# Optimization experiments

Measured on AMD Instinct MI355X. Metric: run time of the kernel, lower is better.

## Reference

```python
import jax, jax.numpy as jnp
import numpy as np

B, L, H = 16, 96, 150
WED, PED = 100, 50
EMB = WED + PED  # 150
WV, TV = 50000, 50


def setup_inputs() -> dict:
    key = jax.random.key(0)
    ks = jax.random.split(key, 16)
    f = lambda k, shape, s=0.1: jax.random.normal(k, shape, dtype=jnp.float32) * s
    return {
        "words_idx_tensor": jax.random.randint(ks[0], (B, L), 0, WV),
        "pos_idx_tensor": jax.random.randint(ks[1], (B, L), 0, TV),
        "max_length": L,
        "word_emb": f(ks[2], (WV, WED)),
        "tag_emb": f(ks[3], (TV, PED)),
        "W_ih0": f(ks[4], (2, 4 * H, EMB)),        # layer 0, both dirs
        "W_ih_rest": f(ks[5], (3, 2, 4 * H, 2 * H)),  # layers 1-3
        "W_hh": f(ks[6], (4, 2, 4 * H, H)),
        "b_ih": f(ks[7], (4, 2, 4 * H)),
        "b_hh": f(ks[8], (4, 2, 4 * H)),
        "w1": jax.random.uniform(ks[9], (1,), jnp.float32, -1.0, 1.0),
        "w2": jax.random.uniform(ks[10], (1,), jnp.float32, -1.0, 1.0),
        "w3": jax.random.uniform(ks[11], (1,), jnp.float32, -1.0, 1.0),
        "w4": jax.random.uniform(ks[12], (1,), jnp.float32, -1.0, 1.0),
        "mlp_w1": f(ks[13], (100, 4 * H)),
        "mlp_b1": jnp.zeros((100,), jnp.float32),
        "mlp_w2": f(ks[14], (1, 100)),
        "mlp_b2": jnp.zeros((1,), jnp.float32),
    }


def _lstm_dir(x, Wih, Whh, bi, bh):
    # x: [B, T, D] -> hidden states [B, T, H]; torch LSTM cell math (gate order i,f,g,o)
    Bx = x.shape[0]
    Hh = Whh.shape[-1]
    pre = jnp.einsum('btd,gd->btg', x, Wih) + bi + bh  # input contribution, [B,T,4H]

    def step(carry, p):
        h, c = carry
        gates = p + h @ Whh.T
        i, fg, g, o = jnp.split(gates, 4, axis=-1)
        i, fg, o = jax.nn.sigmoid(i), jax.nn.sigmoid(fg), jax.nn.sigmoid(o)
        g = jnp.tanh(g)
        c = fg * c + i * g
        h = o * jnp.tanh(c)
        return (h, c), h

    init = (jnp.zeros((Bx, Hh), x.dtype), jnp.zeros((Bx, Hh), x.dtype))
    _, hs = jax.lax.scan(step, init, pre.transpose(1, 0, 2))  # [T,B,H]
    return hs.transpose(1, 0, 2)


def _bilstm(x, W_ih0, W_ih_rest, W_hh, b_ih, b_hh):
    inp = x
    for layer in range(4):  # fixed structural loop over layers
        outs = []
        for d in range(2):  # forward / backward direction
            Wih = W_ih0[d] if layer == 0 else W_ih_rest[layer - 1, d]
            xs = inp if d == 0 else inp[:, ::-1]
            hs = _lstm_dir(xs, Wih, W_hh[layer, d], b_ih[layer, d], b_hh[layer, d])
            outs.append(hs if d == 0 else hs[:, ::-1])
        inp = jnp.concatenate(outs, axis=-1)  # [B,T,2H]
    return inp


def reference(words_idx_tensor, pos_idx_tensor, max_length, word_emb, tag_emb,
              W_ih0, W_ih_rest, W_hh, b_ih, b_hh, w1, w2, w3, w4,
              mlp_w1, mlp_b1, mlp_w2, mlp_b2):
    we = word_emb[words_idx_tensor[:, :max_length]]   # [B,L,WED]
    te = tag_emb[pos_idx_tensor[:, :max_length]]      # [B,L,PED]
    embeds = jnp.concatenate([we, te], axis=-1)       # [B,L,EMB]
    out = _bilstm(embeds, W_ih0, W_ih_rest, W_hh, b_ih, b_hh)  # [B,L,2H]
    Bn, Lm, C = out.shape
    # features[l1, b, l2] = cat(out[b, l1], out[b, l2])  -> [L, B, L, 4H]
    ht = out.transpose(1, 0, 2)  # [L,B,2H]
    head = jnp.broadcast_to(ht[:, :, None, :], (Lm, Bn, Lm, C))
    dep = jnp.broadcast_to(out[None, :, :, :], (Lm, Bn, Lm, C))
    features = jnp.concatenate([head, dep], axis=-1)  # [L,B,L,4H]
    # w1*f + w2*f^2 + w3*f^3 + w4*f^4 via Horner (single fused elementwise pass)
    poly = features * (w1[0] + features * (w2[0] + features * (w3[0] + features * w4[0])))
    h1 = jnp.tanh(poly @ mlp_w1.T + mlp_b1)           # [L,B,L,100]
    edge_scores = h1 @ mlp_w2.T + mlp_b2              # [L,B,L,1]
    return edge_scores
```

## Files before the change

kernel.cpp:

```cpp
#include <hip/hip_runtime.h>

typedef __attribute__((ext_vector_type(8))) _Float16 half8;
typedef __attribute__((ext_vector_type(4))) _Float16 half4;
typedef __attribute__((ext_vector_type(4))) float float4v;

__device__ __forceinline__ float4v mfma16h(half8 a, half8 b, float4v c) {
  return __builtin_amdgcn_mfma_f32_16x16x32_f16(a, b, c, 0, 0, 0);
}

__device__ __forceinline__ half8 cat44h(half4 a, half4 b) {
  half8 r;
  r[0]=a[0]; r[1]=a[1]; r[2]=a[2]; r[3]=a[3];
  r[4]=b[0]; r[5]=b[1]; r[6]=b[2]; r[7]=b[3];
  return r;
}

__device__ __forceinline__ void split_f16(float x, _Float16& hi, _Float16& lo) {
  hi = (_Float16)x;
  lo = (_Float16)(x - (float)hi);
}

#define KLOG2E 1.442695041f
__device__ __forceinline__ float fast_tanh(float x) {
  float z = __builtin_amdgcn_exp2f(2.f * KLOG2E * x);
  return 1.f - 2.f * __builtin_amdgcn_rcpf(1.f + z);
}


__global__ void prep_kernel(
    const float* __restrict__ Wih0,
    const float* __restrict__ WihR,
    const float* __restrict__ Whh,
    const float* __restrict__ bih,
    const float* __restrict__ bhh,
    const float* __restrict__ w1m,
    const float* __restrict__ b1v,
    _Float16* __restrict__ whh_f,
    _Float16* __restrict__ wih_f,
    _Float16* __restrict__ wpr_f,
    float* __restrict__ bsum, float* __restrict__ b1cat)
{
  const int N_whh  = 8 * 40 * 5 * 512;
  const int N_wih0 = 2 * 40 * 5 * 512;
  const int N_wihr = 6 * 40 * 10 * 512;
  const int N_wpr  = 16 * 10 * 512;
  const int N_bs   = 8 * 640;
  const int total  = N_whh + N_wih0 + N_wihr + N_wpr + N_bs + 256;
  for (int i = blockIdx.x * blockDim.x + threadIdx.x; i < total;
       i += gridDim.x * blockDim.x) {
    int idx = i;
    if (idx < N_whh) {
      int e = idx & 7, lane = (idx >> 3) & 63, r = idx >> 9;
      int kc = r % 5; r /= 5; int nt = r % 40; int ld = r / 40;
      int jrow = (nt >> 2) * 16 + (lane & 15);
      int g = (nt & 3) * 150 + jrow;
      int k = 32 * kc + 16 * (e >> 2) + 4 * (lane >> 4) + (e & 3);
      float v = (jrow < 150 && k < 150) ? Whh[((size_t)ld * 600 + g) * 150 + k] : 0.f;
      whh_f[idx] = (_Float16)v;
      continue;
    }
    idx -= N_whh;
    if (idx < N_wih0) {
      int e = idx & 7, lane = (idx >> 3) & 63, r = idx >> 9;
      int kc = r % 5; r /= 5; int nt = r % 40; int dir = r / 40;
      int jrow = (nt >> 2) * 16 + (lane & 15);
      int g = (nt & 3) * 150 + jrow;
      int k = 32 * kc + 16 * (e >> 2) + 4 * (lane >> 4) + (e & 3);
      float v = (jrow < 150 && k < 150) ? Wih0[((size_t)dir * 600 + g) * 150 + k] : 0.f;
      wih_f[idx] = (_Float16)v;
      continue;
    }
    idx -= N_wih0;
    if (idx < N_wihr) {
      int e = idx & 7, lane = (idx >> 3) & 63, r = idx >> 9;
      int kc = r % 10; r /= 10; int nt = r % 40; int ld = r / 40;
      int jrow = (nt >> 2) * 16 + (lane & 15);
      int g = (nt & 3) * 150 + jrow;
      int k = 32 * kc + 16 * (e >> 2) + 4 * (lane >> 4) + (e & 3);
      float v = (jrow < 150 && k < 300) ? WihR[((size_t)ld * 600 + g) * 300 + k] : 0.f;
      wih_f[N_wih0 + idx] = (_Float16)v;
      continue;
    }
    idx -= N_wihr;
    if (idx < N_wpr) {
      int e = idx & 7, lane = (idx >> 3) & 63, r = idx >> 9;
      int kc = r % 10; int nt = r / 10;
      int ko = 16 * nt + (lane & 15);
      int k = 32 * kc + 16 * (e >> 2) + 4 * (lane >> 4) + (e & 3);
      float v = 0.f;
      if (k < 300) {
        if (ko < 100) v = w1m[(size_t)ko * 600 + k];
        else if (ko < 200) v = w1m[(size_t)(ko - 100) * 600 + 300 + k];
      }
      wpr_f[idx] = (_Float16)v;
      continue;
    }
    idx -= N_wpr;
    if (idx < N_bs) {
      int ld = idx / 640, gp = idx - 640 * ld;
      int nt = gp >> 4, lrow = gp & 15;
      int jrow = (nt >> 2) * 16 + lrow;
      int g = (nt & 3) * 150 + jrow;
      bsum[idx] = (jrow < 150) ? bih[ld * 600 + g] + bhh[ld * 600 + g] : 0.f;
      continue;
    }
    idx -= N_bs;
    b1cat[idx] = (idx < 100) ? b1v[idx] : ((idx < 200) ? b1v[idx - 100] : 0.f);
  }
}

__global__ void embed_kernel(const int* __restrict__ widx, const int* __restrict__ pidx,
    const float* __restrict__ wemb, const float* __restrict__ temb,
    _Float16* __restrict__ xa, _Float16* __restrict__ xb)
{
  int row = blockIdx.x;
  int j = threadIdx.x;
  int b = row & 15, t = row >> 4;
  float v = 0.f;
  if (j < 100) v = wemb[(size_t)widx[b * 96 + t] * 100 + j];
  else if (j < 150) v = temb[(size_t)pidx[b * 96 + t] * 50 + (j - 100)];
  size_t o = (size_t)row * 320 + j;
  xa[o] = (_Float16)v;
  if (j >= 300) xb[o] = (_Float16)0.f;
}

template <int KC>
__global__ __launch_bounds__(512) void pregemm_kernel(
    const _Float16* __restrict__ x_h,
    const _Float16* __restrict__ wih_f,
    const float* __restrict__ bsum_l,
    float* __restrict__ pre)
{
  const int t = blockIdx.x, dir = blockIdx.y;
  const int tid = threadIdx.x, wv = tid >> 6, lane = tid & 63;
  const int lrow = lane & 15, lgrp = lane >> 4;
  const _Float16* wf = wih_f + (size_t)dir * 40 * KC * 512;
  float4v acc[5];
#pragma unroll
  for (int tt = 0; tt < 5; ++tt) acc[tt] = (float4v){0.f, 0.f, 0.f, 0.f};
  const size_t arow = ((size_t)t * 16 + lrow) * 320;
#pragma unroll
  for (int kc = 0; kc < KC; ++kc) {
    int co = 32 * kc + 4 * lgrp;
    half8 ah = cat44h(*(const half4*)(x_h + arow + co),
                      *(const half4*)(x_h + arow + co + 16));
#pragma unroll
    for (int tt = 0; tt < 5; ++tt) {
      int nt = 5 * wv + tt;
      const size_t wo = ((size_t)(nt * KC + kc) * 64 + lane) * 8;
      half8 bw = *(const half8*)(wf + wo);
      acc[tt] = mfma16h(ah, bw, acc[tt]);
    }
  }
  float* po = pre + ((size_t)dir * 96 + t) * 16 * 640;
  const float* bs = bsum_l + dir * 640;
#pragma unroll
  for (int tt = 0; tt < 5; ++tt) {
    int g = 16 * (5 * wv + tt) + lrow;
    float bv = bs[g];
#pragma unroll
    for (int jj = 0; jj < 4; ++jj)
      po[(size_t)(4 * lgrp + jj) * 640 + g] = acc[tt][jj] + bv;
  }
}

__global__ __launch_bounds__(640, 1) void scan_kernel(
    const float* __restrict__ pre,
    const _Float16* __restrict__ whh_f,
    _Float16* __restrict__ xo,
    int layer)
{
  const int dir = blockIdx.x;
  const int tid = threadIdx.x, wv = tid >> 6, lane = tid & 63;
  const int lrow = lane & 15, lgrp = lane >> 4;

  __shared__ __align__(16) _Float16 hb[2][16 * 168];

  for (int i = tid; i < 2 * 16 * 168; i += 640)
    (&hb[0][0])[i] = (_Float16)0.f;

  const _Float16* b_base = whh_f + (size_t)(layer * 2 + dir) * 40 * 5 * 512;
  half8 Bw[4][5];
#pragma unroll
  for (int tt = 0; tt < 4; ++tt)
#pragma unroll
    for (int kc = 0; kc < 5; ++kc) {
      size_t o = ((size_t)((4 * wv + tt) * 5 + kc) * 64 + lane) * 8;
      Bw[tt][kc] = *(const half8*)(b_base + o);
    }

  float cst[4] = {0.f, 0.f, 0.f, 0.f};
  const int j = 16 * wv + lrow;
  const int kcj = j >> 5, wj = j & 31;
  const int hoff = kcj * 32 + ((wj >> 2) & 3) * 8 + (wj >> 4) * 4 + (wj & 3);
  const bool jok = (j < 150);

  const int t0 = dir ? 95 : 0;
  const long pinc = dir ? -(16 * 640) : (16 * 640);
  const long xinc = dir ? -(16 * 320) : (16 * 320);
  const float* pt = pre + (size_t)dir * 96 * 16 * 640 + (size_t)t0 * 16 * 640;
  _Float16* xop = xo + ((size_t)t0 * 16 + 4 * lgrp) * 320 + dir * 150 + j;

  float4v pf[4];
#pragma unroll
  for (int tt = 0; tt < 4; ++tt) {
    int gp = 16 * (4 * wv + tt) + lrow;
#pragma unroll
    for (int jj = 0; jj < 4; ++jj)
      pf[tt][jj] = pt[(size_t)(4 * lgrp + jj) * 640 + gp];
  }
  __syncthreads();

#pragma unroll 1
  for (int step = 0; step < 96; ++step) {
    float4v acc[4];
#pragma unroll
    for (int tt = 0; tt < 4; ++tt) acc[tt] = pf[tt];

    const _Float16* hh = hb[step & 1];
#pragma unroll
    for (int kc = 0; kc < 5; ++kc) {
      const int ao = lrow * 168 + kc * 32 + lgrp * 8;
      half8 ah = *(const half8*)(hh + ao);
#pragma unroll
      for (int tt = 0; tt < 4; ++tt)
        acc[tt] = mfma16h(ah, Bw[tt][kc], acc[tt]);
    }

    pt += pinc;
    if (step < 95) {
#pragma unroll
      for (int tt = 0; tt < 4; ++tt) {
        int gp = 16 * (4 * wv + tt) + lrow;
#pragma unroll
        for (int jj = 0; jj < 4; ++jj)
          pf[tt][jj] = pt[(size_t)(4 * lgrp + jj) * 640 + gp];
      }
    }

    _Float16* nhh = hb[(step + 1) & 1];
#pragma unroll
    for (int jj = 0; jj < 4; ++jj) {
      float zi = __builtin_amdgcn_exp2f(-KLOG2E * acc[0][jj]);
      float zf = __builtin_amdgcn_exp2f(-KLOG2E * acc[1][jj]);
      float zg = __builtin_amdgcn_exp2f(2.f * KLOG2E * acc[2][jj]);
      float zo = __builtin_amdgcn_exp2f(-KLOG2E * acc[3][jj]);
      float rf = __builtin_amdgcn_rcpf(1.f + zf);
      float r2 = __builtin_amdgcn_rcpf((1.f + zi) * (zg + 1.f));
      float c = cst[jj] * rf + (zg - 1.f) * r2;
      cst[jj] = c;
      float zc = __builtin_amdgcn_exp2f(2.f * KLOG2E * c);
      float r3 = __builtin_amdgcn_rcpf((1.f + zo) * (zc + 1.f));
      float h = (zc - 1.f) * r3;
      _Float16 hv = (_Float16)h;
      nhh[(4 * lgrp + jj) * 168 + hoff] = hv;
      if (jok) xop[jj * 320] = hv;
    }
    xop += xinc;
    __syncthreads();
  }
}

__global__ void poly_kernel(const _Float16* __restrict__ xi,
    _Float16* __restrict__ po_h, _Float16* __restrict__ po_l,
    const float* __restrict__ w1, const float* __restrict__ w2,
    const float* __restrict__ w3, const float* __restrict__ w4)
{
  int i = blockIdx.x * 256 + threadIdx.x;
  if (i >= 1536 * 320) return;
  float x = (float)xi[i];
  float p = x * (w1[0] + x * (w2[0] + x * (w3[0] + x * w4[0])));
  _Float16 h, l; split_f16(p, h, l);
  po_h[i] = h; po_l[i] = l;
}

__global__ __launch_bounds__(512) void proj_kernel(
    const _Float16* __restrict__ p_h, const _Float16* __restrict__ p_l,
    const _Float16* __restrict__ wpr_f,
    const float* __restrict__ b1cat,
    float* __restrict__ AD)
{
  const int t = blockIdx.x;
  const int tid = threadIdx.x, wv = tid >> 6, lane = tid & 63;
  const int lrow = lane & 15, lgrp = lane >> 4;
  float4v acc[2] = {{0.f, 0.f, 0.f, 0.f}, {0.f, 0.f, 0.f, 0.f}};
  const size_t arow = ((size_t)t * 16 + lrow) * 320;
#pragma unroll
  for (int kc = 0; kc < 10; ++kc) {
    int co = 32 * kc + 4 * lgrp;
    half8 ah = cat44h(*(const half4*)(p_h + arow + co),
                      *(const half4*)(p_h + arow + co + 16));
    half8 al = cat44h(*(const half4*)(p_l + arow + co),
                      *(const half4*)(p_l + arow + co + 16));
#pragma unroll
    for (int tt = 0; tt < 2; ++tt) {
      int nt = 2 * wv + tt;
      size_t wo = ((size_t)(nt * 10 + kc) * 64 + lane) * 8;
      half8 bw = *(const half8*)(wpr_f + wo);
      acc[tt] = mfma16h(ah, bw, acc[tt]);
      acc[tt] = mfma16h(al, bw, acc[tt]);
    }
  }
#pragma unroll
  for (int tt = 0; tt < 2; ++tt) {
    int ko = 16 * (2 * wv + tt) + lrow;
    float bv = b1cat[ko];
#pragma unroll
    for (int jj = 0; jj < 4; ++jj)
      AD[((size_t)t * 16 + 4 * lgrp + jj) * 256 + ko] = acc[tt][jj] + bv;
  }
}

__global__ __launch_bounds__(768) void combine_kernel(
    const float* __restrict__ AD, const float* __restrict__ w2v,
    const float* __restrict__ b2v, float* __restrict__ out)
{
  const int bb = blockIdx.x & 15, lt = blockIdx.x >> 4;
  const int tid = threadIdx.x;
  __shared__ float Dl[100 * 97];
  __shared__ float Al[100 * 9];
  __shared__ float w2s[100];
  for (int i = tid; i < 96 * 32; i += 768) {
    int ld = i >> 5, f4 = i & 31;
    if (f4 < 25) {
      float4v v = *(const float4v*)(AD + ((size_t)ld * 16 + bb) * 256 + 100 + 4 * f4);
      int k0 = 4 * f4;
      Dl[(k0 + 0) * 97 + ld] = v[0];
      Dl[(k0 + 1) * 97 + ld] = v[1];
      Dl[(k0 + 2) * 97 + ld] = v[2];
      Dl[(k0 + 3) * 97 + ld] = v[3];
    }
  }
  for (int i = tid; i < 8 * 32; i += 768) {
    int lh = i >> 5, f4 = i & 31;
    if (f4 < 25) {
      int lseq = lt * 8 + lh;
      float4v v = *(const float4v*)(AD + ((size_t)lseq * 16 + bb) * 256 + 4 * f4);
      int k0 = 4 * f4;
      Al[(k0 + 0) * 9 + lh] = v[0];
      Al[(k0 + 1) * 9 + lh] = v[1];
      Al[(k0 + 2) * 9 + lh] = v[2];
      Al[(k0 + 3) * 9 + lh] = v[3];
    }
  }
  if (tid < 100) w2s[tid] = w2v[tid];
  __syncthreads();
  int lh = tid / 96, ld = tid - 96 * lh;
  float s = 0.f;
#pragma unroll 4
  for (int k = 0; k < 100; ++k) {
    float x = Al[k * 9 + lh] + Dl[k * 97 + ld];
    s += w2s[k] * fast_tanh(x);
  }
  out[((size_t)(lt * 8 + lh) * 16 + bb) * 96 + ld] = s + b2v[0];
}

extern "C" void kernel_launch(void* const* d_in, const int* in_sizes, int n_in,
                              void* d_out, int out_size, void* d_ws, size_t ws_size,
                              hipStream_t stream)
{
  const int*   widx = (const int*)d_in[0];
  const int*   pidx = (const int*)d_in[1];
  const float* wemb = (const float*)d_in[3];
  const float* temb = (const float*)d_in[4];
  const float* Wih0 = (const float*)d_in[5];
  const float* WihR = (const float*)d_in[6];
  const float* Whh  = (const float*)d_in[7];
  const float* bih  = (const float*)d_in[8];
  const float* bhh  = (const float*)d_in[9];
  const float* w1   = (const float*)d_in[10];
  const float* w2   = (const float*)d_in[11];
  const float* w3   = (const float*)d_in[12];
  const float* w4   = (const float*)d_in[13];
  const float* w1m  = (const float*)d_in[14];
  const float* b1v  = (const float*)d_in[15];
  const float* w2m  = (const float*)d_in[16];
  const float* b2v  = (const float*)d_in[17];
  float* out = (float*)d_out;

  char* ws = (char*)d_ws;
  size_t off = 0;
  auto alloc = [&](size_t bytes) -> char* {
    char* p = ws + off;
    off = (off + bytes + 255) & ~(size_t)255;
    return p;
  };
  _Float16* WHH_F = (_Float16*)alloc(819200ull * 2);
  _Float16* WIH_F = (_Float16*)alloc(1433600ull * 2);
  _Float16* WPR_F = (_Float16*)alloc(81920ull * 2);
  float* BSUM = (float*)alloc(5120ull * 4);
  float* B1C  = (float*)alloc(256ull * 4);
  _Float16* XA = (_Float16*)alloc(491520ull * 2);
  _Float16* XB = (_Float16*)alloc(491520ull * 2);
  _Float16* PH = (_Float16*)alloc(491520ull * 2);
  _Float16* PL = (_Float16*)alloc(491520ull * 2);
  float* PRE = (float*)alloc(1966080ull * 4);
  float* AD  = (float*)alloc(1536ull * 256 * 4);

  prep_kernel<<<512, 256, 0, stream>>>(Wih0, WihR, Whh, bih, bhh, w1m, b1v,
      WHH_F, WIH_F, WPR_F, BSUM, B1C);
  embed_kernel<<<1536, 320, 0, stream>>>(widx, pidx, wemb, temb, XA, XB);

  for (int layer = 0; layer < 4; ++layer) {
    const _Float16* xin = (layer & 1) ? XB : XA;
    _Float16* xout = (layer & 1) ? XA : XB;
    const float* bsl = BSUM + layer * 2 * 640;
    if (layer == 0) {
      pregemm_kernel<5><<<dim3(96, 2), 512, 0, stream>>>(xin, WIH_F, bsl, PRE);
    } else {
      size_t wo = 204800ull + (size_t)(layer - 1) * 409600ull;
      pregemm_kernel<10><<<dim3(96, 2), 512, 0, stream>>>(xin, WIH_F + wo, bsl, PRE);
    }
    scan_kernel<<<2, 640, 0, stream>>>(PRE, WHH_F, xout, layer);
  }
  poly_kernel<<<1920, 256, 0, stream>>>(XA, PH, PL, w1, w2, w3, w4);
  proj_kernel<<<96, 512, 0, stream>>>(PH, PL, WPR_F, B1C, AD);
  combine_kernel<<<192, 768, 0, stream>>>(AD, w2m, b2v, out);
}
```

Measured before the change: 580.8 us.

## Prescale LSTM gate weights, vectorize pre-activation layout, double-buffer scan prefetch

```diff
diff --git a/kernel.cpp b/kernel.cpp
--- a/kernel.cpp
+++ b/kernel.cpp
@@ -56,6 +56,7 @@
       int g = (nt & 3) * 150 + jrow;
       int k = 32 * kc + 16 * (e >> 2) + 4 * (lane >> 4) + (e & 3);
       float v = (jrow < 150 && k < 150) ? Whh[((size_t)ld * 600 + g) * 150 + k] : 0.f;
+      v *= ((nt & 3) == 2) ? (2.f * KLOG2E) : (-KLOG2E);
       whh_f[idx] = (_Float16)v;
       continue;
     }
@@ -67,6 +68,7 @@
       int g = (nt & 3) * 150 + jrow;
       int k = 32 * kc + 16 * (e >> 2) + 4 * (lane >> 4) + (e & 3);
       float v = (jrow < 150 && k < 150) ? Wih0[((size_t)dir * 600 + g) * 150 + k] : 0.f;
+      v *= ((nt & 3) == 2) ? (2.f * KLOG2E) : (-KLOG2E);
       wih_f[idx] = (_Float16)v;
       continue;
     }
@@ -78,6 +80,7 @@
       int g = (nt & 3) * 150 + jrow;
       int k = 32 * kc + 16 * (e >> 2) + 4 * (lane >> 4) + (e & 3);
       float v = (jrow < 150 && k < 300) ? WihR[((size_t)ld * 600 + g) * 300 + k] : 0.f;
+      v *= ((nt & 3) == 2) ? (2.f * KLOG2E) : (-KLOG2E);
       wih_f[N_wih0 + idx] = (_Float16)v;
       continue;
     }
@@ -101,7 +104,9 @@
       int nt = gp >> 4, lrow = gp & 15;
       int jrow = (nt >> 2) * 16 + lrow;
       int g = (nt & 3) * 150 + jrow;
-      bsum[idx] = (jrow < 150) ? bih[ld * 600 + g] + bhh[ld * 600 + g] : 0.f;
+      float v = (jrow < 150) ? bih[ld * 600 + g] + bhh[ld * 600 + g] : 0.f;
+      v *= ((nt & 3) == 2) ? (2.f * KLOG2E) : (-KLOG2E);
+      bsum[idx] = v;
       continue;
     }
     idx -= N_bs;
@@ -152,15 +157,17 @@
       acc[tt] = mfma16h(ah, bw, acc[tt]);
     }
   }
-  float* po = pre + ((size_t)dir * 96 + t) * 16 * 640;
+  float* po = pre + (size_t)(dir * 96 + t) * 10240;
   const float* bs = bsum_l + dir * 640;
 #pragma unroll
   for (int tt = 0; tt < 5; ++tt) {
-    int g = 16 * (5 * wv + tt) + lrow;
-    float bv = bs[g];
-#pragma unroll
-    for (int jj = 0; jj < 4; ++jj)
-      po[(size_t)(4 * lgrp + jj) * 640 + g] = acc[tt][jj] + bv;
+    int nt = 5 * wv + tt;
+    float bv = bs[16 * nt + lrow];
+    float4v v;
+#pragma unroll
+    for (int jj = 0; jj < 4; ++jj) v[jj] = acc[tt][jj] + bv;
+    int tid_s = (nt >> 2) * 64 + lgrp * 16 + lrow;
+    *(float4v*)(po + (size_t)tid_s * 16 + (nt & 3) * 4) = v;
   }
 }
 
@@ -174,9 +181,9 @@
   const int tid = threadIdx.x, wv = tid >> 6, lane = tid & 63;
   const int lrow = lane & 15, lgrp = lane >> 4;
 
-  __shared__ __align__(16) _Float16 hb[2][16 * 168];
-
-  for (int i = tid; i < 2 * 16 * 168; i += 640)
+  __shared__ __align__(16) _Float16 hb[2][16 * 172];
+
+  for (int i = tid; i < 2 * 16 * 172; i += 640)
     (&hb[0][0])[i] = (_Float16)0.f;
 
   const _Float16* b_base = whh_f + (size_t)(layer * 2 + dir) * 40 * 5 * 512;
@@ -196,69 +203,60 @@
   const bool jok = (j < 150);
 
   const int t0 = dir ? 95 : 0;
-  const long pinc = dir ? -(16 * 640) : (16 * 640);
+  const long pincv = dir ? -2560 : 2560;
   const long xinc = dir ? -(16 * 320) : (16 * 320);
-  const float* pt = pre + (size_t)dir * 96 * 16 * 640 + (size_t)t0 * 16 * 640;
+  const float4v* pc = (const float4v*)pre + ((size_t)(dir * 96 + t0) * 640 + tid) * 4;
   _Float16* xop = xo + ((size_t)t0 * 16 + 4 * lgrp) * 320 + dir * 150 + j;
 
-  float4v pf[4];
-#pragma unroll
-  for (int tt = 0; tt < 4; ++tt) {
-    int gp = 16 * (4 * wv + tt) + lrow;
-#pragma unroll
-    for (int jj = 0; jj < 4; ++jj)
-      pf[tt][jj] = pt[(size_t)(4 * lgrp + jj) * 640 + gp];
-  }
+  float4v pfA[4], pfB[4];
+#pragma unroll
+  for (int i = 0; i < 4; ++i) pfA[i] = pc[i];
+  pc += pincv;
+#pragma unroll
+  for (int i = 0; i < 4; ++i) pfB[i] = pc[i];
+  pc += pincv;
   __syncthreads();
 
+#define SCAN_STEP(PF, HIN, HOUT)                                          \
+  {                                                                       \
+    _Pragma("unroll")                                                     \
+    for (int kc = 0; kc < 5; ++kc) {                                      \
+      const int ao = lrow * 172 + kc * 32 + lgrp * 8;                     \
+      half8 ah = *(const half8*)((HIN) + ao);                             \
+      _Pragma("unroll")                                                   \
+      for (int tt = 0; tt < 4; ++tt)                                      \
+        PF[tt] = mfma16h(ah, Bw[tt][kc], PF[tt]);                         \
+    }                                                                     \
+    _Pragma("unroll")                                                     \
+    for (int jj = 0; jj < 4; ++jj) {                                      \
+      float zi = __builtin_amdgcn_exp2f(PF[0][jj]);                       \
+      float zf = __builtin_amdgcn_exp2f(PF[1][jj]);                       \
+      float zg = __builtin_amdgcn_exp2f(PF[2][jj]);                       \
+      float zo = __builtin_amdgcn_exp2f(PF[3][jj]);                       \
+      float rf = __builtin_amdgcn_rcpf(1.f + zf);                         \
+      float r2 = __builtin_amdgcn_rcpf((1.f + zi) * (zg + 1.f));          \
+      float c = cst[jj] * rf + (zg - 1.f) * r2;                           \
+      cst[jj] = c;                                                        \
+      float zc = __builtin_amdgcn_exp2f(2.f * KLOG2E * c);                \
+      float r3 = __builtin_amdgcn_rcpf((1.f + zo) * (zc + 1.f));          \
+      float h = (zc - 1.f) * r3;                                          \
+      _Float16 hv = (_Float16)h;                                          \
+      (HOUT)[(4 * lgrp + jj) * 172 + hoff] = hv;                          \
+      if (jok) xop[jj * 320] = hv;                                        \
+    }                                                                     \
+    _Pragma("unroll")                                                     \
+    for (int i = 0; i < 4; ++i) PF[i] = pc[i];                            \
+    pc += pincv;                                                          \
+    xop += xinc;                                                          \
+    __syncthreads();                                                      \
+  }
+
 #pragma unroll 1
-  for (int step = 0; step < 96; ++step) {
-    float4v acc[4];
-#pragma unroll
-    for (int tt = 0; tt < 4; ++tt) acc[tt] = pf[tt];
-
-    const _Float16* hh = hb[step & 1];
-#pragma unroll
-    for (int kc = 0; kc < 5; ++kc) {
-      const int ao = lrow * 168 + kc * 32 + lgrp * 8;
-      half8 ah = *(const half8*)(hh + ao);
-#pragma unroll
-      for (int tt = 0; tt < 4; ++tt)
-        acc[tt] = mfma16h(ah, Bw[tt][kc], acc[tt]);
-    }
-
-    pt += pinc;
-    if (step < 95) {
-#pragma unroll
-      for (int tt = 0; tt < 4; ++tt) {
-        int gp = 16 * (4 * wv + tt) + lrow;
-#pragma unroll
-        for (int jj = 0; jj < 4; ++jj)
-          pf[tt][jj] = pt[(size_t)(4 * lgrp + jj) * 640 + gp];
-      }
-    }
-
-    _Float16* nhh = hb[(step + 1) & 1];
-#pragma unroll
-    for (int jj = 0; jj < 4; ++jj) {
-      float zi = __builtin_amdgcn_exp2f(-KLOG2E * acc[0][jj]);
-      float zf = __builtin_amdgcn_exp2f(-KLOG2E * acc[1][jj]);
-      float zg = __builtin_amdgcn_exp2f(2.f * KLOG2E * acc[2][jj]);
-      float zo = __builtin_amdgcn_exp2f(-KLOG2E * acc[3][jj]);
-      float rf = __builtin_amdgcn_rcpf(1.f + zf);
-      float r2 = __builtin_amdgcn_rcpf((1.f + zi) * (zg + 1.f));
-      float c = cst[jj] * rf + (zg - 1.f) * r2;
-      cst[jj] = c;
-      float zc = __builtin_amdgcn_exp2f(2.f * KLOG2E * c);
-      float r3 = __builtin_amdgcn_rcpf((1.f + zo) * (zc + 1.f));
-      float h = (zc - 1.f) * r3;
-      _Float16 hv = (_Float16)h;
-      nhh[(4 * lgrp + jj) * 168 + hoff] = hv;
-      if (jok) xop[jj * 320] = hv;
-    }
-    xop += xinc;
-    __syncthreads();
-  }
+  for (int s2 = 0; s2 < 48; ++s2) {
+    SCAN_STEP(pfA, hb[0], hb[1]);
+    SCAN_STEP(pfB, hb[1], hb[0]);
+  }
+#undef SCAN_STEP
 }
 
 __global__ void poly_kernel(const _Float16* __restrict__ xi,
```

New measurement: 543.7 us. 1.07x faster.
